# Kernel optimization log

Measured on AMD Instinct MI355X. Metric: run time of the kernel, lower is better.

The kernel has to match this reference:

```python
import jax, jax.numpy as jnp
import numpy as np

HID = 512
POOL = 4096
N_OBJ = 1280
N_REL = 16384
NUM_OBJ_CLS = 151
NUM_REL_CLS = 51


def setup_inputs() -> dict:
    key = jax.random.key(0)
    ks = jax.random.split(key, 12)
    return {
        'edge_ctx': jax.random.normal(ks[0], (N_OBJ, HID), dtype=jnp.float32),
        'union_features': jax.random.normal(ks[1], (N_REL, POOL), dtype=jnp.float32),
        'W_post_emb': jax.random.normal(ks[2], (HID, 2 * HID), dtype=jnp.float32) * (10.0 / np.sqrt(HID)),
        'b_post_emb': jax.random.normal(ks[3], (2 * HID,), dtype=jnp.float32) * 0.01,
        'W_post_cat': jax.random.normal(ks[4], (2 * HID, POOL), dtype=jnp.float32) * 0.02,
        'b_post_cat': jnp.zeros((POOL,), dtype=jnp.float32),
        'W_rel': jax.random.normal(ks[5], (POOL, NUM_REL_CLS), dtype=jnp.float32) * 0.02,
        'b_rel': jnp.zeros((NUM_REL_CLS,), dtype=jnp.float32),
        'freq_table': jax.random.normal(ks[6], (NUM_OBJ_CLS * NUM_OBJ_CLS, NUM_REL_CLS), dtype=jnp.float32),
        'pair_idx': jax.random.randint(ks[7], (N_REL, 2), 0, N_OBJ, dtype=jnp.int32),
        'obj_preds': jax.random.randint(ks[8], (N_OBJ,), 0, NUM_OBJ_CLS, dtype=jnp.int32),
    }


def reference(edge_ctx, union_features, W_post_emb, b_post_emb, W_post_cat,
              b_post_cat, W_rel, b_rel, freq_table, pair_idx, obj_preds):
    # post_emb: [N_obj, 2*hid]; view(N,2,hid) -> head = first hid, tail = last hid
    edge_rep = edge_ctx @ W_post_emb + b_post_emb
    head_rep = edge_rep[:, :HID]   # [N_obj, hid]
    tail_rep = edge_rep[:, HID:]   # [N_obj, hid]

    # gather subject/object reps per relation pair, concat -> [N_rel, 2*hid]
    prod_rep = jnp.concatenate(
        (head_rep[pair_idx[:, 0]], tail_rep[pair_idx[:, 1]]), axis=-1)

    prod_rep = prod_rep @ W_post_cat + b_post_cat        # [N_rel, pool]
    prod_rep = prod_rep * union_features                  # use_vision fuse
    rel_dists = prod_rep @ W_rel + b_rel                  # [N_rel, num_rel]

    # frequency bias: Embedding over [num_obj^2, num_rel] indexed by label pair
    bias_idx = obj_preds[pair_idx[:, 0]] * NUM_OBJ_CLS + obj_preds[pair_idx[:, 1]]
    rel_dists = rel_dists + freq_table[bias_idx]
    return rel_dists
```

## Files before the change

kernel.cpp:

```cpp
#include <hip/hip_runtime.h>

#define HID 512
#define POOL 4096
#define N_OBJ 1280
#define N_REL 16384
#define NOC 151
#define NRC 51
#define KSPLIT 4

typedef _Float16 half_t;
typedef half_t h16x8 __attribute__((ext_vector_type(8)));
typedef float f32x4 __attribute__((ext_vector_type(4)));

#define LDSTR 72

__global__ __launch_bounds__(256) void kt_transpose(
    const float* __restrict__ src, half_t* __restrict__ dst, int K, int N)
{
    __shared__ __align__(16) half_t Ts[64 * LDSTR];
    const int kb = blockIdx.x * 64, nb = blockIdx.y * 64;
    const int t = threadIdx.x;
    const int kr = t >> 4;
    const int nc = (t & 15) * 4;
#pragma unroll
    for (int p = 0; p < 4; ++p) {
        float4 v = *(const float4*)(src + (size_t)(kb + kr + 16 * p) * N + nb + nc);
        Ts[(nc + 0) * LDSTR + kr + 16 * p] = (half_t)v.x;
        Ts[(nc + 1) * LDSTR + kr + 16 * p] = (half_t)v.y;
        Ts[(nc + 2) * LDSTR + kr + 16 * p] = (half_t)v.z;
        Ts[(nc + 3) * LDSTR + kr + 16 * p] = (half_t)v.w;
    }
    __syncthreads();
    const int n = t >> 2, kk = (t & 3) * 16;
    half_t* d = dst + (size_t)(nb + n) * K + kb + kk;
    *(h16x8*)(d)     = *(const h16x8*)&Ts[n * LDSTR + kk];
    *(h16x8*)(d + 8) = *(const h16x8*)&Ts[n * LDSTR + kk + 8];
}

__global__ __launch_bounds__(256) void k1_edge_rep(
    const float* __restrict__ edge_ctx,
    const half_t* __restrict__ Wet,
    const float* __restrict__ be,
    half_t* __restrict__ E)
{
    __shared__ __align__(16) half_t As[64 * LDSTR];
    __shared__ __align__(16) half_t Bs[64 * LDSTR];

    const int m0 = blockIdx.x * 64;
    const int n0 = blockIdx.y * 64;
    const int t = threadIdx.x;
    const int wave = t >> 6, lane = t & 63;
    const int quad = lane >> 4, l16 = lane & 15;

    const int ar  = t >> 2;
    const int akb = (t & 3) * 16;

    f32x4 acc[4] = {};

    for (int k0 = 0; k0 < HID; k0 += 64) {
        {
            const float* src = edge_ctx + (size_t)(m0 + ar) * HID + k0 + akb;
#pragma unroll
            for (int i = 0; i < 2; ++i) {
                float4 va = *(const float4*)(src + 8 * i);
                float4 vb = *(const float4*)(src + 8 * i + 4);
                h16x8 o;
                o[0] = (half_t)va.x; o[1] = (half_t)va.y;
                o[2] = (half_t)va.z; o[3] = (half_t)va.w;
                o[4] = (half_t)vb.x; o[5] = (half_t)vb.y;
                o[6] = (half_t)vb.z; o[7] = (half_t)vb.w;
                *(h16x8*)&As[ar * LDSTR + akb + 8 * i] = o;
            }
        }
        {
            const half_t* src = Wet + (size_t)(n0 + ar) * HID + k0 + akb;
            *(h16x8*)&Bs[ar * LDSTR + akb]     = *(const h16x8*)(src);
            *(h16x8*)&Bs[ar * LDSTR + akb + 8] = *(const h16x8*)(src + 8);
        }
        __syncthreads();
#pragma unroll
        for (int s = 0; s < 2; ++s) {
            h16x8 a = *(const h16x8*)&As[(wave * 16 + l16) * LDSTR + s * 32 + quad * 8];
#pragma unroll
            for (int nt = 0; nt < 4; ++nt) {
                h16x8 b = *(const h16x8*)&Bs[(nt * 16 + l16) * LDSTR + s * 32 + quad * 8];
                acc[nt] = __builtin_amdgcn_mfma_f32_16x16x32_f16(a, b, acc[nt], 0, 0, 0);
            }
        }
        __syncthreads();
    }
#pragma unroll
    for (int nt = 0; nt < 4; ++nt) {
        int n = n0 + nt * 16 + l16;
        float bias = be[n];
#pragma unroll
        for (int r = 0; r < 4; ++r) {
            int m = m0 + wave * 16 + quad * 4 + r;
            E[(size_t)m * 1024 + n] = (half_t)(acc[nt][r] + bias);
        }
    }
}

__global__ __launch_bounds__(256) void k2_ht(
    const half_t* __restrict__ E,
    const half_t* __restrict__ Wct,
    const float* __restrict__ bcat,
    half_t* __restrict__ Hws,
    half_t* __restrict__ Tws)
{
    __shared__ __align__(16) half_t As[64 * LDSTR];
    __shared__ __align__(16) half_t Bs[64 * LDSTR];

    const int z  = blockIdx.z;
    const int m0 = blockIdx.x * 64;
    const int n0 = blockIdx.y * 64;
    const int t = threadIdx.x;
    const int wave = t >> 6, lane = t & 63;
    const int quad = lane >> 4, l16 = lane & 15;

    const int ar  = t >> 2;
    const int akb = (t & 3) * 16;

    f32x4 acc[4] = {};

    for (int k0 = 0; k0 < HID; k0 += 64) {
        {
            const half_t* src = E + (size_t)(m0 + ar) * 1024 + z * 512 + k0 + akb;
            *(h16x8*)&As[ar * LDSTR + akb]     = *(const h16x8*)(src);
            *(h16x8*)&As[ar * LDSTR + akb + 8] = *(const h16x8*)(src + 8);
        }
        {
            const half_t* src = Wct + (size_t)(n0 + ar) * 1024 + z * 512 + k0 + akb;
            *(h16x8*)&Bs[ar * LDSTR + akb]     = *(const h16x8*)(src);
            *(h16x8*)&Bs[ar * LDSTR + akb + 8] = *(const h16x8*)(src + 8);
        }
        __syncthreads();
#pragma unroll
        for (int s = 0; s < 2; ++s) {
            h16x8 a = *(const h16x8*)&As[(wave * 16 + l16) * LDSTR + s * 32 + quad * 8];
#pragma unroll
            for (int nt = 0; nt < 4; ++nt) {
                h16x8 b = *(const h16x8*)&Bs[(nt * 16 + l16) * LDSTR + s * 32 + quad * 8];
                acc[nt] = __builtin_amdgcn_mfma_f32_16x16x32_f16(a, b, acc[nt], 0, 0, 0);
            }
        }
        __syncthreads();
    }
    half_t* outp = z ? Tws : Hws;
#pragma unroll
    for (int nt = 0; nt < 4; ++nt) {
        int n = n0 + nt * 16 + l16;
        float bias = z ? 0.0f : bcat[n];
#pragma unroll
        for (int r = 0; r < 4; ++r) {
            int m = m0 + wave * 16 + quad * 4 + r;
            outp[(size_t)m * POOL + n] = (half_t)(acc[nt][r] + bias);
        }
    }
}

__global__ __launch_bounds__(256) void k2b_wt(
    const float* __restrict__ Wrel, half_t* __restrict__ Wt)
{
    int k = blockIdx.x * 256 + threadIdx.x;
#pragma unroll 8
    for (int n = 0; n < 64; ++n) {
        float v = (n < NRC) ? Wrel[(size_t)k * NRC + n] : 0.0f;
        Wt[(size_t)n * POOL + k] = (half_t)v;
    }
}

__global__ __launch_bounds__(256) void k3_main(
    const float* __restrict__ unionf,
    const half_t* __restrict__ Hws,
    const half_t* __restrict__ Tws,
    const half_t* __restrict__ Wt,
    const float* __restrict__ brel,
    const float* __restrict__ freq,
    const int* __restrict__ pair_idx,
    const int* __restrict__ obj_preds,
    float* __restrict__ out)
{
    __shared__ __align__(16) half_t As[64 * LDSTR];
    __shared__ __align__(16) half_t Bs[64 * LDSTR];

    const int R0 = blockIdx.x * 64;
    const int kbase = blockIdx.y * (POOL / KSPLIT);
    const int t = threadIdx.x;
    const int wave = t >> 6, lane = t & 63;
    const int quad = lane >> 4, l16 = lane & 15;

    const int ar  = t >> 2;
    const int akb = (t & 3) * 16;

    const int2 pr = *(const int2*)(pair_idx + 2 * (R0 + ar));
    const half_t* Hrow = Hws + (size_t)pr.x * POOL;
    const half_t* Trow = Tws + (size_t)pr.y * POOL;
    const float*  urow = unionf + (size_t)(R0 + ar) * POOL;

    f32x4 acc[4] = {};

    for (int k0 = kbase; k0 < kbase + POOL / KSPLIT; k0 += 64) {
#pragma unroll
        for (int i = 0; i < 2; ++i) {
            h16x8 hv = *(const h16x8*)(Hrow + k0 + akb + 8 * i);
            h16x8 tv = *(const h16x8*)(Trow + k0 + akb + 8 * i);
            float4 ua = *(const float4*)(urow + k0 + akb + 8 * i);
            float4 ub = *(const float4*)(urow + k0 + akb + 8 * i + 4);
            h16x8 o;
            o[0] = (half_t)(((float)hv[0] + (float)tv[0]) * ua.x);
            o[1] = (half_t)(((float)hv[1] + (float)tv[1]) * ua.y);
            o[2] = (half_t)(((float)hv[2] + (float)tv[2]) * ua.z);
            o[3] = (half_t)(((float)hv[3] + (float)tv[3]) * ua.w);
            o[4] = (half_t)(((float)hv[4] + (float)tv[4]) * ub.x);
            o[5] = (half_t)(((float)hv[5] + (float)tv[5]) * ub.y);
            o[6] = (half_t)(((float)hv[6] + (float)tv[6]) * ub.z);
            o[7] = (half_t)(((float)hv[7] + (float)tv[7]) * ub.w);
            *(h16x8*)&As[ar * LDSTR + akb + 8 * i] = o;
        }
        {
            const half_t* src = Wt + (size_t)ar * POOL + k0 + akb;
            *(h16x8*)&Bs[ar * LDSTR + akb]     = *(const h16x8*)(src);
            *(h16x8*)&Bs[ar * LDSTR + akb + 8] = *(const h16x8*)(src + 8);
        }
        __syncthreads();
#pragma unroll
        for (int s = 0; s < 2; ++s) {
            h16x8 a = *(const h16x8*)&As[(wave * 16 + l16) * LDSTR + s * 32 + quad * 8];
#pragma unroll
            for (int nt = 0; nt < 4; ++nt) {
                h16x8 b = *(const h16x8*)&Bs[(nt * 16 + l16) * LDSTR + s * 32 + quad * 8];
                acc[nt] = __builtin_amdgcn_mfma_f32_16x16x32_f16(a, b, acc[nt], 0, 0, 0);
            }
        }
        __syncthreads();
    }
    const bool first = (blockIdx.y == 0);
#pragma unroll
    for (int r = 0; r < 4; ++r) {
        int grow = R0 + wave * 16 + quad * 4 + r;
        const float* frow = nullptr;
        if (first) {
            int2 p = *(const int2*)(pair_idx + 2 * grow);
            frow = freq + (size_t)(obj_preds[p.x] * NOC + obj_preds[p.y]) * NRC;
        }
#pragma unroll
        for (int nt = 0; nt < 4; ++nt) {
            int n = nt * 16 + l16;
            if (n < NRC) {
                float v = acc[nt][r];
                if (first) v += brel[n] + frow[n];
                atomicAdd(&out[(size_t)grow * NRC + n], v);
            }
        }
    }
}

extern "C" void kernel_launch(void* const* d_in, const int* in_sizes, int n_in,
                              void* d_out, int out_size, void* d_ws, size_t ws_size,
                              hipStream_t stream) {
    const float* edge_ctx  = (const float*)d_in[0];
    const float* unionf    = (const float*)d_in[1];
    const float* We        = (const float*)d_in[2];
    const float* be        = (const float*)d_in[3];
    const float* Wc        = (const float*)d_in[4];
    const float* bcat      = (const float*)d_in[5];
    const float* Wrel      = (const float*)d_in[6];
    const float* brel      = (const float*)d_in[7];
    const float* freq      = (const float*)d_in[8];
    const int*   pair_idx  = (const int*)d_in[9];
    const int*   obj_preds = (const int*)d_in[10];
    float* out = (float*)d_out;

    char* ws = (char*)d_ws;
    half_t* E   = (half_t*)(ws);
    half_t* H   = (half_t*)(ws + 2621440);
    half_t* T   = (half_t*)(ws + 13107200);
    half_t* Wt  = (half_t*)(ws + 23592960);
    half_t* Wct = (half_t*)(ws + 24117248);
    half_t* Wet = (half_t*)(ws + 32505856);

    hipMemsetAsync(out, 0, (size_t)out_size * sizeof(float), stream);

    kt_transpose<<<dim3(HID / 64, 1024 / 64), 256, 0, stream>>>(We, Wet, HID, 1024);
    kt_transpose<<<dim3(1024 / 64, POOL / 64), 256, 0, stream>>>(Wc, Wct, 1024, POOL);
    k2b_wt<<<POOL / 256, 256, 0, stream>>>(Wrel, Wt);
    k1_edge_rep<<<dim3(N_OBJ / 64, 1024 / 64), 256, 0, stream>>>(edge_ctx, Wet, be, E);
    k2_ht<<<dim3(N_OBJ / 64, POOL / 64, 2), 256, 0, stream>>>(E, Wct, bcat, H, T);
    k3_main<<<dim3(N_REL / 64, KSPLIT), 256, 0, stream>>>(unionf, H, T, Wt, brel, freq,
                                                          pair_idx, obj_preds, out);
}
```

Before: 478.5 us.

## Enlarge k2_ht GEMM tile to 128x128 and coalesce W_rel transpose via LDS

The head/tail projection GEMM moves from 64x64 to 128x128 tiles, with each wave computing a 64x64 sub-tile of 4x4 MFMA accumulators. This raises operand reuse from LDS and cuts global reloads of E and Wct. The W_rel transpose now stages a 64-row chunk in shared memory so it can issue 16-byte coalesced half-precision writes instead of strided scalar stores. In exchange, the GEMM uses more registers per thread and launches fewer blocks (640 versus 2560), which may lower occupancy.

```diff
diff --git a/kernel.cpp b/kernel.cpp
--- a/kernel.cpp
+++ b/kernel.cpp
@@ -108,53 +108,61 @@
     half_t* __restrict__ Hws,
     half_t* __restrict__ Tws)
 {
-    __shared__ __align__(16) half_t As[64 * LDSTR];
-    __shared__ __align__(16) half_t Bs[64 * LDSTR];
+    __shared__ __align__(16) half_t As[128 * LDSTR];
+    __shared__ __align__(16) half_t Bs[128 * LDSTR];
 
     const int z  = blockIdx.z;
-    const int m0 = blockIdx.x * 64;
-    const int n0 = blockIdx.y * 64;
+    const int m0 = blockIdx.x * 128;
+    const int n0 = blockIdx.y * 128;
     const int t = threadIdx.x;
     const int wave = t >> 6, lane = t & 63;
     const int quad = lane >> 4, l16 = lane & 15;
-
-    const int ar  = t >> 2;
-    const int akb = (t & 3) * 16;
-
-    f32x4 acc[4] = {};
+    const int wr = wave >> 1, wc = wave & 1;
+
+    const int srow = t >> 3;
+    const int sc   = (t & 7) * 8;
+
+    f32x4 acc[4][4] = {};
 
     for (int k0 = 0; k0 < HID; k0 += 64) {
-        {
-            const half_t* src = E + (size_t)(m0 + ar) * 1024 + z * 512 + k0 + akb;
-            *(h16x8*)&As[ar * LDSTR + akb]     = *(const h16x8*)(src);
-            *(h16x8*)&As[ar * LDSTR + akb + 8] = *(const h16x8*)(src + 8);
-        }
-        {
-            const half_t* src = Wct + (size_t)(n0 + ar) * 1024 + z * 512 + k0 + akb;
-            *(h16x8*)&Bs[ar * LDSTR + akb]     = *(const h16x8*)(src);
-            *(h16x8*)&Bs[ar * LDSTR + akb + 8] = *(const h16x8*)(src + 8);
+#pragma unroll
+        for (int p = 0; p < 4; ++p) {
+            int row = srow + 32 * p;
+            *(h16x8*)&As[row * LDSTR + sc] =
+                *(const h16x8*)(E + (size_t)(m0 + row) * 1024 + z * 512 + k0 + sc);
+            *(h16x8*)&Bs[row * LDSTR + sc] =
+                *(const h16x8*)(Wct + (size_t)(n0 + row) * 1024 + z * 512 + k0 + sc);
         }
         __syncthreads();
 #pragma unroll
         for (int s = 0; s < 2; ++s) {
-            h16x8 a = *(const h16x8*)&As[(wave * 16 + l16) * LDSTR + s * 32 + quad * 8];
-#pragma unroll
-            for (int nt = 0; nt < 4; ++nt) {
-                h16x8 b = *(const h16x8*)&Bs[(nt * 16 + l16) * LDSTR + s * 32 + quad * 8];
-                acc[nt] = __builtin_amdgcn_mfma_f32_16x16x32_f16(a, b, acc[nt], 0, 0, 0);
-            }
+            h16x8 a[4], b[4];
+#pragma unroll
+            for (int i = 0; i < 4; ++i) {
+                a[i] = *(const h16x8*)&As[(wr * 64 + i * 16 + l16) * LDSTR + s * 32 + quad * 8];
+                b[i] = *(const h16x8*)&Bs[(wc * 64 + i * 16 + l16) * LDSTR + s * 32 + quad * 8];
+            }
+#pragma unroll
+            for (int ri = 0; ri < 4; ++ri)
+#pragma unroll
+                for (int ci = 0; ci < 4; ++ci)
+                    acc[ri][ci] = __builtin_amdgcn_mfma_f32_16x16x32_f16(
+                        a[ri], b[ci], acc[ri][ci], 0, 0, 0);
         }
         __syncthreads();
     }
     half_t* outp = z ? Tws : Hws;
 #pragma unroll
-    for (int nt = 0; nt < 4; ++nt) {
-        int n = n0 + nt * 16 + l16;
+    for (int ci = 0; ci < 4; ++ci) {
+        int n = n0 + wc * 64 + ci * 16 + l16;
         float bias = z ? 0.0f : bcat[n];
 #pragma unroll
-        for (int r = 0; r < 4; ++r) {
-            int m = m0 + wave * 16 + quad * 4 + r;
-            outp[(size_t)m * POOL + n] = (half_t)(acc[nt][r] + bias);
+        for (int ri = 0; ri < 4; ++ri) {
+#pragma unroll
+            for (int r = 0; r < 4; ++r) {
+                int m = m0 + wr * 64 + ri * 16 + quad * 4 + r;
+                outp[(size_t)m * POOL + n] = (half_t)(acc[ri][ci][r] + bias);
+            }
         }
     }
 }
@@ -162,12 +170,22 @@
 __global__ __launch_bounds__(256) void k2b_wt(
     const float* __restrict__ Wrel, half_t* __restrict__ Wt)
 {
-    int k = blockIdx.x * 256 + threadIdx.x;
-#pragma unroll 8
-    for (int n = 0; n < 64; ++n) {
-        float v = (n < NRC) ? Wrel[(size_t)k * NRC + n] : 0.0f;
-        Wt[(size_t)n * POOL + k] = (half_t)v;
-    }
+    __shared__ float Ls[64 * NRC];
+    const int kb = blockIdx.x * 64;
+    const int t = threadIdx.x;
+    for (int f = t; f < 64 * NRC; f += 256)
+        Ls[f] = Wrel[(size_t)kb * NRC + f];
+    __syncthreads();
+    const int n = t >> 2, kc = t & 3;
+    h16x8 o0, o1;
+#pragma unroll
+    for (int e = 0; e < 8; ++e) {
+        o0[e] = (n < NRC) ? (half_t)Ls[(kc * 16 + e) * NRC + n] : (half_t)0.0f;
+        o1[e] = (n < NRC) ? (half_t)Ls[(kc * 16 + 8 + e) * NRC + n] : (half_t)0.0f;
+    }
+    half_t* d = Wt + (size_t)n * POOL + kb + kc * 16;
+    *(h16x8*)(d)     = o0;
+    *(h16x8*)(d + 8) = o1;
 }
 
 __global__ __launch_bounds__(256) void k3_main(
@@ -284,9 +302,9 @@
 
     kt_transpose<<<dim3(HID / 64, 1024 / 64), 256, 0, stream>>>(We, Wet, HID, 1024);
     kt_transpose<<<dim3(1024 / 64, POOL / 64), 256, 0, stream>>>(Wc, Wct, 1024, POOL);
-    k2b_wt<<<POOL / 256, 256, 0, stream>>>(Wrel, Wt);
+    k2b_wt<<<POOL / 64, 256, 0, stream>>>(Wrel, Wt);
     k1_edge_rep<<<dim3(N_OBJ / 64, 1024 / 64), 256, 0, stream>>>(edge_ctx, Wet, be, E);
-    k2_ht<<<dim3(N_OBJ / 64, POOL / 64, 2), 256, 0, stream>>>(E, Wct, bcat, H, T);
+    k2_ht<<<dim3(N_OBJ / 128, POOL / 128, 2), 256, 0, stream>>>(E, Wct, bcat, H, T);
     k3_main<<<dim3(N_REL / 64, KSPLIT), 256, 0, stream>>>(unionf, H, T, Wt, brel, freq,
                                                           pair_idx, obj_preds, out);
 }
```

New measurement: 471.3 us. No clear change (-1.5%).
